# Performance work log

Hardware: AMD Instinct MI355X
Metric: run time of the kernel (lower is better)

## Reference

```python
import jax, jax.numpy as jnp
import numpy as np

L, H, NH, NKV, HD, I, V, B, S = 18, 640, 4, 1, 256, 2048, 32768, 1, 1024
WINDOW = 512
EPS = 1e-6
THETA_G = 1000000.0
THETA_L = 10000.0


def _rms(x, w):
    # Gemma RMSNorm: x / rms(x) * (1 + w)
    var = jnp.mean(jnp.square(x), axis=-1, keepdims=True)
    return x * jax.lax.rsqrt(var + EPS) * (1.0 + w)


def _rope_tables(theta):
    inv = 1.0 / (theta ** (jnp.arange(0, HD, 2, dtype=jnp.float32) / HD))
    f = jnp.arange(S, dtype=jnp.float32)[:, None] * inv[None, :]
    emb = jnp.concatenate([f, f], axis=-1)  # [S, HD]
    return jnp.cos(emb), jnp.sin(emb)


def _rope(x, cos, sin):
    # x: [B, S, n, HD]
    x1, x2 = jnp.split(x, 2, axis=-1)
    rot = jnp.concatenate([-x2, x1], axis=-1)
    return x * cos[None, :, None, :] + rot * sin[None, :, None, :]


def setup_inputs() -> dict:
    key = jax.random.key(0)
    ks = jax.random.split(key, 16)
    r = lambda k, sh: jax.random.normal(k, sh, jnp.float32) * 0.02
    return {
        'input_ids': jax.random.randint(ks[0], (B, S), 0, V, jnp.int32),
        'is_full': jnp.array([(i + 1) % 6 == 0 for i in range(L)]),
        'embed': r(ks[1], (V, H)),
        'wq': r(ks[2], (L, H, NH * HD)),
        'wk': r(ks[3], (L, H, NKV * HD)),
        'wv': r(ks[4], (L, H, NKV * HD)),
        'wo': r(ks[5], (L, NH * HD, H)),
        'qn': jnp.zeros((L, HD)), 'kn': jnp.zeros((L, HD)),
        'ln1': jnp.zeros((L, H)), 'ln2': jnp.zeros((L, H)),
        'ln3': jnp.zeros((L, H)), 'ln4': jnp.zeros((L, H)),
        'wg': r(ks[6], (L, H, I)), 'wu': r(ks[7], (L, H, I)),
        'wd': r(ks[8], (L, I, H)),
        'norm_w': jnp.zeros((H,)),
    }


def _forward(embed, wq, wk, wv, wo, qn, kn, ln1, ln2, ln3, ln4, wg, wu, wd,
             norm_w, input_ids, is_full):
    cos_g, sin_g = _rope_tables(THETA_G)
    cos_l, sin_l = _rope_tables(THETA_L)
    pos = jnp.arange(S)
    causal = pos[:, None] >= pos[None, :]
    sliding = causal & ((pos[:, None] - pos[None, :]) < WINDOW)
    scale = HD ** -0.5
    grp = NH // NKV

    h = embed[input_ids] * jnp.asarray(H ** 0.5, embed.dtype)  # [B,S,H]

    def body(h, xs):
        (wq_, wk_, wv_, wo_, qn_, kn_, l1, l2, l3, l4, wg_, wu_, wd_, full) = xs
        cos = jnp.where(full, cos_g, cos_l)
        sin = jnp.where(full, sin_g, sin_l)
        mask = jnp.where(full, causal, sliding)
        x = _rms(h, l1)
        q = (x @ wq_).reshape(B, S, NH, HD)
        k = (x @ wk_).reshape(B, S, NKV, HD)
        v = (x @ wv_).reshape(B, S, NKV, HD)
        q = _rope(_rms(q, qn_), cos, sin)
        k = _rope(_rms(k, kn_), cos, sin)
        qg = q.reshape(B, S, NKV, grp, HD)
        scores = jnp.einsum('bqngd,bsnd->bngqs', qg, k) * scale
        scores = jnp.where(mask[None, None, None], scores, -1e30)
        attn = jax.nn.softmax(scores, axis=-1)
        o = jnp.einsum('bngqs,bsnd->bqngd', attn, v).reshape(B, S, NH * HD)
        h = h + _rms(o @ wo_, l2)               # post_attention_layernorm then residual
        x = _rms(h, l3)                          # pre_feedforward_layernorm
        mlp = (jax.nn.gelu(x @ wg_, approximate=True) * (x @ wu_)) @ wd_  # GeGLU
        h = h + _rms(mlp, l4)                    # post_feedforward_layernorm then residual
        return h, None

    h, _ = jax.lax.scan(body, h, (wq, wk, wv, wo, qn, kn, ln1, ln2, ln3, ln4, wg, wu, wd, is_full))
    h = _rms(h, norm_w)
    # lm_head tied to embed_tokens; final_logit_softcapping = 0.0 (disabled)
    return jnp.einsum('bsh,vh->bsv', h, embed)


def reference(input_ids, is_full, embed, wq, wk, wv, wo, qn, kn,
              ln1, ln2, ln3, ln4, wg, wu, wd, norm_w):
    return _forward(embed, wq, wk, wv, wo, qn, kn, ln1, ln2, ln3, ln4,
                    wg, wu, wd, norm_w, input_ids, is_full)
```

## Files before the change

### kernel.cpp

```cpp
#include <hip/hip_runtime.h>


typedef unsigned short u16;
typedef __attribute__((ext_vector_type(4))) float f32x4;
typedef __attribute__((ext_vector_type(8))) short bf16x8;

#define DEV static __device__ __forceinline__

DEV u16 f2bf(float f) {
  union { float f; unsigned u; } x; x.f = f;
  unsigned r = x.u + 0x7fffu + ((x.u >> 16) & 1u);
  return (u16)(r >> 16);
}

#define GLOAD16(gp, lp) __builtin_amdgcn_global_load_lds( \
    (const __attribute__((address_space(1))) void*)(gp), \
    (__attribute__((address_space(3))) void*)(lp), 16, 0, 0)

DEV float blockSum(float v, float* red) {
#pragma unroll
  for (int o = 32; o; o >>= 1) v += __shfl_down(v, o);
  int lane = threadIdx.x & 63, wid = threadIdx.x >> 6;
  if (lane == 0) red[wid] = v;
  __syncthreads();
  float s = red[0] + red[1] + red[2] + red[3];
  __syncthreads();
  return s;
}

DEV float blockMax(float v, float* red) {
#pragma unroll
  for (int o = 32; o; o >>= 1) v = fmaxf(v, __shfl_down(v, o));
  int lane = threadIdx.x & 63, wid = threadIdx.x >> 6;
  if (lane == 0) red[wid] = v;
  __syncthreads();
  float s = fmaxf(fmaxf(red[0], red[1]), fmaxf(red[2], red[3]));
  __syncthreads();
  return s;
}

DEV void cstore(float* C, size_t i, float v) { C[i] = v; }
DEV void cstore(u16* C, size_t i, float v) { C[i] = f2bf(v); }

template <typename CT, int GEGLU, int BKT>
__global__ __launch_bounds__(256) void gemm_nt(
    const u16* __restrict__ A, int lda, long sA,
    const u16* __restrict__ B, int ldb, long sB,
    CT* __restrict__ C, int ldc, long sC,
    int K, float alpha, int kmode, int nshift, int ksplit) {
  constexpr int DB = 128 * BKT;
  __shared__ __align__(16) u16 As[2 * DB];
  __shared__ __align__(16) u16 Bs[2 * DB];
  const int m0 = blockIdx.y * 128;
  int n0;
  if (nshift == -1) n0 = blockIdx.x * 128;
  else if (nshift == -2) { n0 = blockIdx.x * 128; if (n0 > m0) return; }
  else { n0 = m0 - nshift + blockIdx.x * 128; if (n0 < 0) return; }
  int klo = 0, khi = K;
  if (kmode == 1) { klo = m0 - 512; if (klo < 0) klo = 0; khi = m0 + 128; if (khi > K) khi = K; }
  else if (kmode == 2) { khi = m0 + 128; if (khi > K) khi = K; }
  else if (kmode == 3) { int kl = K / ksplit; klo = blockIdx.z * kl; khi = klo + kl; }
  A += (long)blockIdx.z * sA;
  B += (long)blockIdx.z * sB;

  const int t = threadIdx.x;
  const int l = t & 63, w = t >> 6;
  const int wr = w >> 1, wc = w & 1;
  const int lr = l & 15, lk = l >> 4;
  const int srow = (BKT == 64) ? (t >> 3) : (t >> 2);
  const int scolx = (BKT == 64) ? (((t & 7) ^ (srow & 7)) << 3)
                                : (((t & 3) ^ (srow & 3)) << 3);
  const u16* Ag = A + (size_t)(m0 + srow) * lda + scolx;
  const u16* Bg = B + (size_t)(n0 + srow) * ldb + scolx;
  const int nsteps = (khi - klo) / BKT;

  auto stage = [&](int db, int k0) {
    u16* al = As + db * DB + w * 512;
    u16* bl = Bs + db * DB + w * 512;
    if constexpr (BKT == 64) {
#pragma unroll
      for (int p = 0; p < 4; ++p) {
        GLOAD16(Ag + k0 + (size_t)(32 * p) * lda, al + p * 2048);
        GLOAD16(Bg + k0 + (size_t)(32 * p) * ldb, bl + p * 2048);
      }
    } else {
#pragma unroll
      for (int p = 0; p < 2; ++p) {
        GLOAD16(Ag + k0 + (size_t)(64 * p) * lda, al + p * 2048);
        GLOAD16(Bg + k0 + (size_t)(64 * p) * ldb, bl + p * 2048);
      }
    }
  };

  stage(0, klo);
  f32x4 acc[4][4] = {};

  for (int s = 0; s < nsteps; ++s) {
    __syncthreads();
    const int db = s & 1;
    if (s + 1 < nsteps) stage(db ^ 1, klo + (s + 1) * BKT);
    const u16* Ab = As + db * DB;
    const u16* Bb = Bs + db * DB;
    if constexpr (BKT == 64) {
      const int axr = lr & 7;
      bf16x8 af[2][4], bfr[2][4];
#pragma unroll
      for (int kk = 0; kk < 2; ++kk)
#pragma unroll
        for (int i = 0; i < 4; ++i) {
          af[kk][i]  = *(const bf16x8*)&Ab[(wr * 64 + i * 16 + lr) * 64 + (((kk * 4 + lk) ^ axr) << 3)];
          bfr[kk][i] = *(const bf16x8*)&Bb[(wc * 64 + i * 16 + lr) * 64 + (((kk * 4 + lk) ^ axr) << 3)];
        }
#pragma unroll
      for (int kk = 0; kk < 2; ++kk)
#pragma unroll
        for (int mi = 0; mi < 4; ++mi)
#pragma unroll
          for (int ni = 0; ni < 4; ++ni)
            acc[mi][ni] = __builtin_amdgcn_mfma_f32_16x16x32_bf16(af[kk][mi], bfr[kk][ni], acc[mi][ni], 0, 0, 0);
    } else {
      const int key = lr & 3;
      bf16x8 af[4], bfr[4];
#pragma unroll
      for (int i = 0; i < 4; ++i) {
        af[i]  = *(const bf16x8*)&Ab[(wr * 64 + i * 16 + lr) * 32 + ((lk ^ key) << 3)];
        bfr[i] = *(const bf16x8*)&Bb[(wc * 64 + i * 16 + lr) * 32 + ((lk ^ key) << 3)];
      }
#pragma unroll
      for (int mi = 0; mi < 4; ++mi)
#pragma unroll
        for (int ni = 0; ni < 4; ++ni)
          acc[mi][ni] = __builtin_amdgcn_mfma_f32_16x16x32_bf16(af[mi], bfr[ni], acc[mi][ni], 0, 0, 0);
    }
  }

  C += (long)blockIdx.z * sC;
  if (GEGLU) {
#pragma unroll
    for (int mi = 0; mi < 4; ++mi) {
      int row = m0 + wr * 64 + mi * 16 + lk * 4;
#pragma unroll
      for (int np = 0; np < 2; ++np) {
        int col = (n0 + wc * 64) / 2 + np * 16 + lr;
#pragma unroll
        for (int j = 0; j < 4; ++j) {
          float g = acc[mi][2 * np][j], u = acc[mi][2 * np + 1][j];
          float z = 0.7978845608028654f * (g + 0.044715f * g * g * g);
          float th = 2.0f / (1.0f + __expf(-2.0f * z)) - 1.0f;
          cstore(C, (size_t)(row + j) * ldc + col, 0.5f * g * (1.0f + th) * u);
        }
      }
    }
  } else {
#pragma unroll
    for (int mi = 0; mi < 4; ++mi) {
      int row = m0 + wr * 64 + mi * 16 + lk * 4;
#pragma unroll
      for (int ni = 0; ni < 4; ++ni) {
        int col = n0 + wc * 64 + ni * 16 + lr;
#pragma unroll
        for (int j = 0; j < 4; ++j)
          cstore(C, (size_t)(row + j) * ldc + col, acc[mi][ni][j] * alpha);
      }
    }
  }
}

__global__ void conv_bf16_kernel(const float* __restrict__ in, u16* __restrict__ out, long n4) {
  for (long i = (long)blockIdx.x * blockDim.x + threadIdx.x; i < n4; i += (long)gridDim.x * blockDim.x) {
    float4 v = ((const float4*)in)[i];
    ushort4 o4 = { f2bf(v.x), f2bf(v.y), f2bf(v.z), f2bf(v.w) };
    ((ushort4*)out)[i] = o4;
  }
}

__global__ void gather_rms_kernel(const int* __restrict__ ids, const float* __restrict__ embed,
                                  const float* __restrict__ w, float* __restrict__ h,
                                  u16* __restrict__ x) {
  __shared__ float red[8];
  const int s = blockIdx.x, t = threadIdx.x;
  const float* src = embed + (size_t)ids[s] * 640;
  const float scale = sqrtf(640.0f);
  float hv[3];
  float ss = 0.0f;
#pragma unroll
  for (int i = 0; i < 3; ++i) {
    int c = t + i * 256;
    float v = (c < 640) ? src[c] * scale : 0.0f;
    hv[i] = v; ss += v * v;
  }
  ss = blockSum(ss, red);
  const float sc = rsqrtf(ss * (1.0f / 640.0f) + 1e-6f);
#pragma unroll
  for (int i = 0; i < 3; ++i) {
    int c = t + i * 256;
    if (c < 640) {
      h[(size_t)s * 640 + c] = hv[i];
      x[(size_t)s * 640 + c] = f2bf(hv[i] * sc * (1.0f + w[c]));
    }
  }
}

__global__ void fused_add_norm(float* __restrict__ h, const float* __restrict__ t1,
                               int nsl, const float* __restrict__ wa,
                               const float* __restrict__ wn, u16* __restrict__ xout) {
  __shared__ float red[8];
  const int row = blockIdx.x, t = threadIdx.x;
  float ts[3], hv[3];
  float ss = 0.0f;
#pragma unroll
  for (int i = 0; i < 3; ++i) {
    int c = t + i * 256;
    float v = 0.0f;
    if (c < 640) {
      v = t1[(size_t)row * 640 + c];
      for (int z = 1; z < nsl; ++z) v += t1[(size_t)z * 655360 + (size_t)row * 640 + c];
    }
    ts[i] = v; ss += v * v;
  }
  ss = blockSum(ss, red);
  const float s1 = rsqrtf(ss * (1.0f / 640.0f) + 1e-6f);
  float ss2 = 0.0f;
#pragma unroll
  for (int i = 0; i < 3; ++i) {
    int c = t + i * 256;
    float v = 0.0f;
    if (c < 640) v = h[(size_t)row * 640 + c] + ts[i] * s1 * (1.0f + wa[c]);
    hv[i] = v; ss2 += v * v;
  }
  ss2 = blockSum(ss2, red);
  const float s2 = rsqrtf(ss2 * (1.0f / 640.0f) + 1e-6f);
#pragma unroll
  for (int i = 0; i < 3; ++i) {
    int c = t + i * 256;
    if (c < 640) {
      h[(size_t)row * 640 + c] = hv[i];
      xout[(size_t)row * 640 + c] = f2bf(hv[i] * s2 * (1.0f + wn[c]));
    }
  }
}

__global__ void rope_tables_kernel(float* cg, float* sg, float* cl, float* sl) {
  int s = blockIdx.x, t = threadIdx.x;
  float e = -(float)t * (1.0f / 128.0f);
  float ag = (float)s * expf(e * logf(1000000.0f));
  float al = (float)s * expf(e * logf(10000.0f));
  cg[s * 128 + t] = cosf(ag); sg[s * 128 + t] = sinf(ag);
  cl[s * 128 + t] = cosf(al); sl[s * 128 + t] = sinf(al);
}

__global__ void rope_fused(const float* __restrict__ qkvf, const float* __restrict__ qn,
                           const float* __restrict__ kn, u16* __restrict__ qb,
                           u16* __restrict__ kb, u16* __restrict__ vt,
                           const float* __restrict__ ct, const float* __restrict__ st) {
  __shared__ float red[8];
  __shared__ float sh[256];
  const int s = blockIdx.x, hh = blockIdx.y, t = threadIdx.x;
  if (hh == 5) {
    vt[(size_t)t * 1024 + s] = f2bf(qkvf[(size_t)s * 1536 + 1280 + t]);
    return;
  }
  const float* src = qkvf + (size_t)s * 1536 + hh * 256;
  const float* nw = (hh == 4) ? kn : qn;
  float x = src[t];
  float ss = blockSum(x * x, red);
  float n = x * rsqrtf(ss * (1.0f / 256.0f) + 1e-6f) * (1.0f + nw[t]);
  sh[t] = n;
  __syncthreads();
  float cosv = ct[s * 128 + (t & 127)];
  float sinv = st[s * 128 + (t & 127)];
  float partner = (t < 128) ? -sh[t + 128] : sh[t - 128];
  u16 r = f2bf(n * cosv + partner * sinv);
  if (hh == 4) kb[(size_t)s * 256 + t] = r;
  else qb[((size_t)hh * 1024 + s) * 256 + t] = r;
}

__global__ void softmax_kernel(const float* __restrict__ sc, u16* __restrict__ P, int mode) {
  __shared__ float red[8];
  const int i = blockIdx.x, hh = blockIdx.y, t = threadIdx.x;
  const float* row = sc + ((size_t)hh * 1024 + i) * 1024;
  u16* prow = P + ((size_t)hh * 1024 + i) * 1024;
  const int m0 = i & ~127;
  int lo = 0, wlo = 0;
  if (mode) {
    lo = i - 511; if (lo < 0) lo = 0;
    wlo = m0 - 512; if (wlo < 0) wlo = 0;
  }
  const int whi = m0 + 127;
  float m = -1e30f;
  for (int j = lo + t; j <= i; j += 256) m = fmaxf(m, row[j]);
  m = blockMax(m, red);
  float sum = 0.0f;
  for (int j = lo + t; j <= i; j += 256) sum += __expf(row[j] - m);
  sum = blockSum(sum, red);
  float inv = 1.0f / sum;
  for (int j = wlo + t; j <= whi; j += 256) {
    float v = (j >= lo && j <= i) ? __expf(row[j] - m) * inv : 0.0f;
    prow[j] = f2bf(v);
  }
}

__global__ void transpose7_kernel(
    const float* s0, const float* s1, const float* s2, const float* s3,
    const float* s4, const float* s5, const float* s6,
    u16* d0, u16* d1, u16* d2, u16* d3, u16* d45, u16* d6) {
  __shared__ float tile[64][65];
  int b = blockIdx.x;
  const float* src; u16* dst; int K, N, idx, ilv = 0;
  if (b < 160)       { src = s0; dst = d0;  K = 640;  N = 1024; idx = b; }
  else if (b < 200)  { src = s1; dst = d1;  K = 640;  N = 256;  idx = b - 160; }
  else if (b < 240)  { src = s2; dst = d2;  K = 640;  N = 256;  idx = b - 200; }
  else if (b < 400)  { src = s3; dst = d3;  K = 1024; N = 640;  idx = b - 240; }
  else if (b < 720)  { src = s4; dst = d45; K = 640;  N = 2048; idx = b - 400;  ilv = 1; }
  else if (b < 1040) { src = s5; dst = d45; K = 640;  N = 2048; idx = b - 720;  ilv = 2; }
  else               { src = s6; dst = d6;  K = 2048; N = 640;  idx = b - 1040; }
  int tn = N >> 6;
  int kt = idx / tn, nt = idx % tn;
  int t = threadIdx.x;
  int lr = t >> 4, lc = (t & 15) * 4;
#pragma unroll
  for (int i = 0; i < 4; ++i) {
    float4 v = *(const float4*)&src[(size_t)(kt * 64 + lr + i * 16) * N + nt * 64 + lc];
    tile[lr + i * 16][lc] = v.x; tile[lr + i * 16][lc + 1] = v.y;
    tile[lr + i * 16][lc + 2] = v.z; tile[lr + i * 16][lc + 3] = v.w;
  }
  __syncthreads();
  int wn = t >> 3, wk8 = (t & 7) * 8;
#pragma unroll
  for (int i = 0; i < 2; ++i) {
    int gcol = nt * 64 + wn + i * 32;
    int drow = ilv ? ((gcol >> 4) * 32 + ((ilv == 2) ? 16 : 0) + (gcol & 15)) : gcol;
    u16 tmp[8];
#pragma unroll
    for (int j = 0; j < 8; ++j) tmp[j] = f2bf(tile[wk8 + j][wn + i * 32]);
    *(int4*)&dst[(size_t)drow * K + kt * 64 + wk8] = *(int4*)tmp;
  }
}

extern "C" void kernel_launch(void* const* d_in, const int* in_sizes, int n_in,
                              void* d_out, int out_size, void* d_ws, size_t ws_size,
                              hipStream_t stream) {
  (void)in_sizes; (void)n_in; (void)out_size; (void)ws_size;
  const int*   ids   = (const int*)d_in[0];
  const float* embed = (const float*)d_in[2];
  const float* wq    = (const float*)d_in[3];
  const float* wk    = (const float*)d_in[4];
  const float* wv    = (const float*)d_in[5];
  const float* wo    = (const float*)d_in[6];
  const float* qn    = (const float*)d_in[7];
  const float* kn    = (const float*)d_in[8];
  const float* ln1   = (const float*)d_in[9];
  const float* ln2   = (const float*)d_in[10];
  const float* ln3   = (const float*)d_in[11];
  const float* ln4   = (const float*)d_in[12];
  const float* wg    = (const float*)d_in[13];
  const float* wu    = (const float*)d_in[14];
  const float* wd    = (const float*)d_in[15];
  const float* nw    = (const float*)d_in[16];
  float* out = (float*)d_out;

  const int S = 1024, H = 640, NH = 4, HD = 256, I = 2048, V = 32768;

  unsigned char* p = (unsigned char*)d_ws;
  auto alloc = [&](size_t b) { void* r = (void*)p; p += (b + 255) & ~(size_t)255; return r; };
  u16*   wqkvT = (u16*)alloc((size_t)1536 * 640 * 2);
  u16*   woT   = (u16*)alloc((size_t)640 * 1024 * 2);
  u16*   wguT  = (u16*)alloc((size_t)4096 * 640 * 2);
  u16*   wdT   = (u16*)alloc((size_t)640 * 2048 * 2);
  u16*   embT  = (u16*)alloc((size_t)V * H * 2);
  float* h     = (float*)alloc((size_t)S * H * 4);
  u16*   x     = (u16*)alloc((size_t)S * H * 2);
  float* qkvf  = (float*)alloc((size_t)S * 1536 * 4);
  u16*   qb    = (u16*)alloc((size_t)NH * S * HD * 2);
  u16*   kb    = (u16*)alloc((size_t)S * HD * 2);
  u16*   vt    = (u16*)alloc((size_t)HD * S * 2);
  float* scp   = (float*)alloc((size_t)NH * S * S * 4);
  u16*   P     = (u16*)alloc((size_t)NH * S * S * 2);
  u16*   o     = (u16*)alloc((size_t)S * NH * HD * 2);
  float* t1    = (float*)alloc((size_t)4 * S * H * 4);
  u16*   mg    = (u16*)alloc((size_t)S * I * 2);
  u16*   hn    = (u16*)alloc((size_t)S * H * 2);
  float* cg    = (float*)alloc((size_t)S * 128 * 4);
  float* sg    = (float*)alloc((size_t)S * 128 * 4);
  float* cl    = (float*)alloc((size_t)S * 128 * 4);
  float* sl2   = (float*)alloc((size_t)S * 128 * 4);

  rope_tables_kernel<<<S, 128, 0, stream>>>(cg, sg, cl, sl2);
  conv_bf16_kernel<<<2048, 256, 0, stream>>>(embed, embT, (long)V * H / 4);
  gather_rms_kernel<<<S, 256, 0, stream>>>(ids, embed, ln1, h, x);

  for (int l = 0; l < 18; ++l) {
    bool full = ((l + 1) % 6) == 0;

    transpose7_kernel<<<1360, 256, 0, stream>>>(
        wq + (size_t)l * H * 1024, wk + (size_t)l * H * 256, wv + (size_t)l * H * 256,
        wo + (size_t)l * 1024 * H, wg + (size_t)l * H * I, wu + (size_t)l * H * I,
        wd + (size_t)l * I * H,
        wqkvT, wqkvT + (size_t)1024 * 640, wqkvT + (size_t)1280 * 640, woT, wguT, wdT);

    gemm_nt<float, 0, 64><<<dim3(12, 8, 1), 256, 0, stream>>>(
        x, H, 0, wqkvT, H, 0, qkvf, 1536, 0, H, 1.0f, 0, -1, 1);
    rope_fused<<<dim3(S, 6), 256, 0, stream>>>(qkvf, qn + l * HD, kn + l * HD, qb, kb, vt,
                                               full ? cg : cl, full ? sg : sl2);
    if (full)
      gemm_nt<float, 0, 64><<<dim3(8, 8, NH), 256, 0, stream>>>(
          qb, HD, (long)S * HD, kb, HD, 0, scp, S, (long)S * S, HD, 0.0625f, 0, -2, 1);
    else
      gemm_nt<float, 0, 64><<<dim3(5, 8, NH), 256, 0, stream>>>(
          qb, HD, (long)S * HD, kb, HD, 0, scp, S, (long)S * S, HD, 0.0625f, 0, 512, 1);
    softmax_kernel<<<dim3(S, NH), 256, 0, stream>>>(scp, P, full ? 0 : 1);
    gemm_nt<u16, 0, 64><<<dim3(2, 8, NH), 256, 0, stream>>>(
        P, S, (long)S * S, vt, S, 0, o, NH * HD, HD, S, 1.0f, full ? 2 : 1, -1, 1);
    gemm_nt<float, 0, 64><<<dim3(5, 8, 2), 256, 0, stream>>>(
        o, NH * HD, 0, woT, NH * HD, 0, t1, H, (long)S * H, NH * HD, 1.0f, 3, -1, 2);
    fused_add_norm<<<S, 256, 0, stream>>>(h, t1, 2, ln2 + l * H, ln3 + l * H, x);

    gemm_nt<u16, 1, 64><<<dim3(32, 8, 1), 256, 0, stream>>>(
        x, H, 0, wguT, H, 0, mg, I, 0, H, 1.0f, 0, -1, 1);
    gemm_nt<float, 0, 64><<<dim3(5, 8, 4), 256, 0, stream>>>(
        mg, I, 0, wdT, I, 0, t1, H, (long)S * H, I, 1.0f, 3, -1, 4);
    fused_add_norm<<<S, 256, 0, stream>>>(h, t1, 4, ln4 + l * H,
                                          (l == 17) ? nw : ln1 + (l + 1) * H,
                                          (l == 17) ? hn : x);
  }

  gemm_nt<float, 0, 32><<<dim3(V / 128, 8, 1), 256, 0, stream>>>(
      hn, H, 0, embT, H, 0, out, V, 0, H, 1.0f, 0, -1, 1);
}
```

Measured before the change: 2.078 ms.

## Replace score GEMM, softmax and PV GEMM with fused flash attention kernel

Attention no longer materializes fp32 scores and bf16 probabilities in global memory. A single online-softmax kernel computes QK^T, masking, softmax and PV per 64-row query block, with each wave handling 16 rows and loading K and V straight from global memory. The swizzle key for the BKT=32 GEMM path is also changed to use row>>1, which targets LDS bank conflicts in the lm_head GEMM. The tradeoff is a grid of only 64 blocks per layer with no LDS staging of K/V, so occupancy and memory reuse may be poor.

```diff
diff --git a/kernel.cpp b/kernel.cpp
--- a/kernel.cpp
+++ b/kernel.cpp
@@ -24,17 +24,6 @@
   if (lane == 0) red[wid] = v;
   __syncthreads();
   float s = red[0] + red[1] + red[2] + red[3];
-  __syncthreads();
-  return s;
-}
-
-DEV float blockMax(float v, float* red) {
-#pragma unroll
-  for (int o = 32; o; o >>= 1) v = fmaxf(v, __shfl_down(v, o));
-  int lane = threadIdx.x & 63, wid = threadIdx.x >> 6;
-  if (lane == 0) red[wid] = v;
-  __syncthreads();
-  float s = fmaxf(fmaxf(red[0], red[1]), fmaxf(red[2], red[3]));
   __syncthreads();
   return s;
 }
@@ -69,7 +58,7 @@
   const int lr = l & 15, lk = l >> 4;
   const int srow = (BKT == 64) ? (t >> 3) : (t >> 2);
   const int scolx = (BKT == 64) ? (((t & 7) ^ (srow & 7)) << 3)
-                                : (((t & 3) ^ (srow & 3)) << 3);
+                                : (((t & 3) ^ ((srow >> 1) & 3)) << 3);
   const u16* Ag = A + (size_t)(m0 + srow) * lda + scolx;
   const u16* Bg = B + (size_t)(n0 + srow) * ldb + scolx;
   const int nsteps = (khi - klo) / BKT;
@@ -119,7 +108,7 @@
           for (int ni = 0; ni < 4; ++ni)
             acc[mi][ni] = __builtin_amdgcn_mfma_f32_16x16x32_bf16(af[kk][mi], bfr[kk][ni], acc[mi][ni], 0, 0, 0);
     } else {
-      const int key = lr & 3;
+      const int key = (lr >> 1) & 3;
       bf16x8 af[4], bfr[4];
 #pragma unroll
       for (int i = 0; i < 4; ++i) {
@@ -164,6 +153,117 @@
       }
     }
   }
+}
+
+__global__ __launch_bounds__(256) void flash_attn(
+    const u16* __restrict__ qb, const u16* __restrict__ kb,
+    const u16* __restrict__ vt, u16* __restrict__ o, int isfull) {
+  __shared__ __align__(16) u16 Ps[4][16][80];
+  const int m0 = blockIdx.x * 64, z = blockIdx.y;
+  const int t = threadIdx.x;
+  const int l = t & 63, w = t >> 6;
+  const int lr = l & 15, lk = l >> 4;
+  const int mw = m0 + w * 16;
+
+  bf16x8 afq[8];
+  {
+    const u16* qp = qb + (size_t)(z * 1024 + mw + lr) * 256 + lk * 8;
+#pragma unroll
+    for (int kk = 0; kk < 8; ++kk) afq[kk] = *(const bf16x8*)(qp + kk * 32);
+  }
+
+  int klo = 0;
+  if (!isfull) { klo = mw - 511; if (klo < 0) klo = 0; klo &= ~63; }
+  const int ntiles = (mw + 16 - klo + 63) >> 6;
+  const int qrow_base = mw + (l >> 4) * 4;
+
+  float m_run[4] = {-1e30f, -1e30f, -1e30f, -1e30f};
+  float l_run[4] = {};
+  f32x4 oacc[16] = {};
+
+  for (int tile = 0; tile < ntiles; ++tile) {
+    const int k0 = klo + tile * 64;
+    f32x4 sacc[4] = {};
+#pragma unroll
+    for (int kk = 0; kk < 8; ++kk) {
+      bf16x8 bfr[4];
+#pragma unroll
+      for (int ni = 0; ni < 4; ++ni)
+        bfr[ni] = *(const bf16x8*)&kb[(size_t)(k0 + ni * 16 + lr) * 256 + kk * 32 + lk * 8];
+#pragma unroll
+      for (int ni = 0; ni < 4; ++ni)
+        sacc[ni] = __builtin_amdgcn_mfma_f32_16x16x32_bf16(afq[kk], bfr[ni], sacc[ni], 0, 0, 0);
+    }
+
+    float sv[4][4], mx[4], rs[4], sf[4];
+#pragma unroll
+    for (int j = 0; j < 4; ++j) mx[j] = -1e30f;
+#pragma unroll
+    for (int ni = 0; ni < 4; ++ni)
+#pragma unroll
+      for (int j = 0; j < 4; ++j) {
+        int q = qrow_base + j, s = k0 + ni * 16 + lr;
+        bool valid = (s <= q) && (isfull || s >= q - 511);
+        float v = valid ? sacc[ni][j] * 0.0625f : -1e30f;
+        sv[ni][j] = v;
+        mx[j] = fmaxf(mx[j], v);
+      }
+#pragma unroll
+    for (int j = 0; j < 4; ++j) {
+#pragma unroll
+      for (int d = 1; d < 16; d <<= 1) mx[j] = fmaxf(mx[j], __shfl_xor(mx[j], d));
+      float mn = fmaxf(m_run[j], mx[j]);
+      sf[j] = __expf(m_run[j] - mn);
+      m_run[j] = mn;
+      rs[j] = 0.0f;
+    }
+    float pv[4][4];
+#pragma unroll
+    for (int ni = 0; ni < 4; ++ni)
+#pragma unroll
+      for (int j = 0; j < 4; ++j) {
+        float p = (sv[ni][j] <= -1e29f) ? 0.0f : __expf(sv[ni][j] - m_run[j]);
+        pv[ni][j] = p;
+        rs[j] += p;
+      }
+#pragma unroll
+    for (int j = 0; j < 4; ++j) {
+#pragma unroll
+      for (int d = 1; d < 16; d <<= 1) rs[j] += __shfl_xor(rs[j], d);
+      l_run[j] = l_run[j] * sf[j] + rs[j];
+    }
+#pragma unroll
+    for (int nd = 0; nd < 16; ++nd)
+#pragma unroll
+      for (int j = 0; j < 4; ++j) oacc[nd][j] *= sf[j];
+
+#pragma unroll
+    for (int ni = 0; ni < 4; ++ni)
+#pragma unroll
+      for (int j = 0; j < 4; ++j)
+        Ps[w][(l >> 4) * 4 + j][ni * 16 + (l & 15)] = f2bf(pv[ni][j]);
+    bf16x8 ap[2];
+#pragma unroll
+    for (int kk = 0; kk < 2; ++kk)
+      ap[kk] = *(const bf16x8*)&Ps[w][lr][kk * 32 + lk * 8];
+
+#pragma unroll
+    for (int nd = 0; nd < 16; ++nd)
+#pragma unroll
+      for (int kk = 0; kk < 2; ++kk) {
+        bf16x8 bv = *(const bf16x8*)&vt[(size_t)(nd * 16 + lr) * 1024 + k0 + kk * 32 + lk * 8];
+        oacc[nd] = __builtin_amdgcn_mfma_f32_16x16x32_bf16(ap[kk], bv, oacc[nd], 0, 0, 0);
+      }
+  }
+
+#pragma unroll
+  for (int nd = 0; nd < 16; ++nd)
+#pragma unroll
+    for (int j = 0; j < 4; ++j) {
+      int q = qrow_base + j;
+      int d = z * 256 + nd * 16 + (l & 15);
+      o[(size_t)q * 1024 + d] = f2bf(oacc[nd][j] / l_run[j]);
+    }
 }
 
 __global__ void conv_bf16_kernel(const float* __restrict__ in, u16* __restrict__ out, long n4) {
@@ -273,31 +373,6 @@
   u16 r = f2bf(n * cosv + partner * sinv);
   if (hh == 4) kb[(size_t)s * 256 + t] = r;
   else qb[((size_t)hh * 1024 + s) * 256 + t] = r;
-}
-
-__global__ void softmax_kernel(const float* __restrict__ sc, u16* __restrict__ P, int mode) {
-  __shared__ float red[8];
-  const int i = blockIdx.x, hh = blockIdx.y, t = threadIdx.x;
-  const float* row = sc + ((size_t)hh * 1024 + i) * 1024;
-  u16* prow = P + ((size_t)hh * 1024 + i) * 1024;
-  const int m0 = i & ~127;
-  int lo = 0, wlo = 0;
-  if (mode) {
-    lo = i - 511; if (lo < 0) lo = 0;
-    wlo = m0 - 512; if (wlo < 0) wlo = 0;
-  }
-  const int whi = m0 + 127;
-  float m = -1e30f;
-  for (int j = lo + t; j <= i; j += 256) m = fmaxf(m, row[j]);
-  m = blockMax(m, red);
-  float sum = 0.0f;
-  for (int j = lo + t; j <= i; j += 256) sum += __expf(row[j] - m);
-  sum = blockSum(sum, red);
-  float inv = 1.0f / sum;
-  for (int j = wlo + t; j <= whi; j += 256) {
-    float v = (j >= lo && j <= i) ? __expf(row[j] - m) * inv : 0.0f;
-    prow[j] = f2bf(v);
-  }
 }
 
 __global__ void transpose7_kernel(
@@ -374,8 +449,6 @@
   u16*   qb    = (u16*)alloc((size_t)NH * S * HD * 2);
   u16*   kb    = (u16*)alloc((size_t)S * HD * 2);
   u16*   vt    = (u16*)alloc((size_t)HD * S * 2);
-  float* scp   = (float*)alloc((size_t)NH * S * S * 4);
-  u16*   P     = (u16*)alloc((size_t)NH * S * S * 2);
   u16*   o     = (u16*)alloc((size_t)S * NH * HD * 2);
   float* t1    = (float*)alloc((size_t)4 * S * H * 4);
   u16*   mg    = (u16*)alloc((size_t)S * I * 2);
@@ -402,15 +475,7 @@
         x, H, 0, wqkvT, H, 0, qkvf, 1536, 0, H, 1.0f, 0, -1, 1);
     rope_fused<<<dim3(S, 6), 256, 0, stream>>>(qkvf, qn + l * HD, kn + l * HD, qb, kb, vt,
                                                full ? cg : cl, full ? sg : sl2);
-    if (full)
-      gemm_nt<float, 0, 64><<<dim3(8, 8, NH), 256, 0, stream>>>(
-          qb, HD, (long)S * HD, kb, HD, 0, scp, S, (long)S * S, HD, 0.0625f, 0, -2, 1);
-    else
-      gemm_nt<float, 0, 64><<<dim3(5, 8, NH), 256, 0, stream>>>(
-          qb, HD, (long)S * HD, kb, HD, 0, scp, S, (long)S * S, HD, 0.0625f, 0, 512, 1);
-    softmax_kernel<<<dim3(S, NH), 256, 0, stream>>>(scp, P, full ? 0 : 1);
-    gemm_nt<u16, 0, 64><<<dim3(2, 8, NH), 256, 0, stream>>>(
-        P, S, (long)S * S, vt, S, 0, o, NH * HD, HD, S, 1.0f, full ? 2 : 1, -1, 1);
+    flash_attn<<<dim3(16, NH), 256, 0, stream>>>(qb, kb, vt, o, full ? 1 : 0);
     gemm_nt<float, 0, 64><<<dim3(5, 8, 2), 256, 0, stream>>>(
         o, NH * HD, 0, woT, NH * HD, 0, t1, H, (long)S * H, NH * HD, 1.0f, 3, -1, 2);
     fused_add_norm<<<S, 256, 0, stream>>>(h, t1, 2, ln2 + l * H, ln3 + l * H, x);
```

New measurement: 3.327 ms. 60.2% more time.
